# Kernel optimization log

Measured on AMD Instinct MI355X. Metric: run time of the kernel, lower is better.

Reference implementation:

```python
import jax, jax.numpy as jnp
import numpy as np

B, T, V, K = 8, 256, 16, 8
L_SRL, L_VN = 66, 40  # PropBank / VerbNet label inventory sizes


def setup_inputs() -> dict:
    key = jax.random.key(0)
    ks = jax.random.split(key, 7)
    log_srl = jax.random.normal(ks[0], (B, T, T, L_SRL), jnp.float32)
    log_vn = jax.random.normal(ks[1], (B, T, T, L_VN), jnp.float32)
    v_label = jax.random.randint(ks[2], (B, V), 0, T)          # predicate token positions
    v_l = jax.random.randint(ks[3], (B,), 1, V + 1)            # num predicates per example
    orig_l = jax.random.randint(ks[4], (B,), T // 2, T + 1)    # original seq lengths
    semlink = jax.random.randint(ks[5], (B, V, 2, K), 0, L_VN) # [.,.,0,:]=srl label ids, [.,.,1,:]=vn label ids
    semlink_l = jax.random.randint(ks[6], (B, V), 0, K + 1)    # num semlink constraints per predicate
    return {"log_srl": log_srl, "log_vn": log_vn, "v_label": v_label,
            "v_l": v_l, "orig_l": orig_l, "semlink": semlink, "semlink_l": semlink_l}


def reference(log_srl, log_vn, v_label, v_l, orig_l, semlink, semlink_l):
    # log_srl: [B,T,T,L_srl], log_vn: [B,T,T,L_vn]
    Bn, Tn = log_srl.shape[0], log_srl.shape[1]
    Vn, Kn = v_label.shape[1], semlink.shape[-1]
    b = jnp.arange(Bn)[:, None]
    # Gather predicate rows: [B,V,T,L]
    sel_srl = log_srl[b, v_label]
    sel_vn = log_vn[b, v_label]
    # batch_index1_select: gather along label axis with semlink label ids -> [B,V,T,K]
    r_idx = semlink[:, :, 0, :]  # [B,V,K]
    a_idx = semlink[:, :, 1, :]
    g_r = jnp.take_along_axis(sel_srl, r_idx[:, :, None, :], axis=3)
    g_a = jnp.take_along_axis(sel_vn, a_idx[:, :, None, :], axis=3)
    diff = jnp.abs(g_r - g_a)  # [B,V,T,K]
    # masks: semlink length (len_to_mask), valid predicates, valid tokens (:orig_l)
    k_mask = jnp.arange(Kn)[None, None, :] < semlink_l[:, :, None]   # [B,V,K]
    v_mask = jnp.arange(Vn)[None, :] < v_l[:, None]                  # [B,V]
    t_mask = jnp.arange(Tn)[None, :] < orig_l[:, None]               # [B,T]
    mask = (k_mask[:, :, None, :] & v_mask[:, :, None, None] & t_mask[:, None, :, None])
    loss = jnp.sum(jnp.where(mask, diff, 0.0))
    num_prop = jnp.sum(v_l).astype(log_srl.dtype)  # use_gold_predicate == 1 normalizer
    return loss / num_prop
```

## Files before the change

### kernel.cpp

```cpp
#include <hip/hip_runtime.h>

#define Bn   8
#define Tn   256
#define Vn   16
#define Kn   8
#define LSRL 66
#define LVN  40

#define SUM_SCALE 1073741824.0
#define SUM_MASK  ((1ULL << 56) - 1)
#define CNT_ONE   (1ULL << 56)
#define POISON    0xAAAAAAAAAAAAAAAAULL
#define POISON_END_CNT (((POISON >> 56) + 128) & 255ULL)

__global__ __launch_bounds__(256)
void semlink_onepass_kernel(const float* __restrict__ log_srl,
                            const float* __restrict__ log_vn,
                            const int*   __restrict__ v_label,
                            const int*   __restrict__ v_l,
                            const int*   __restrict__ orig_l,
                            const int*   __restrict__ semlink,
                            const int*   __restrict__ semlink_l,
                            unsigned long long* __restrict__ acc,
                            float*       __restrict__ out) {
    const int bv = blockIdx.x;
    const int b  = bv >> 4;
    const int v  = bv & 15;
    const int t  = threadIdx.x;
    const int lane = t & 63;
    const int wid  = t >> 6;

    __shared__ int s_idx[2 * Kn];
    __shared__ int s_meta[4];

    if (t < 2 * Kn) s_idx[t] = semlink[bv * (2 * Kn) + t];
    if (t == 0) {
        s_meta[0] = v_label[bv];
        s_meta[1] = semlink_l[bv];
        s_meta[2] = v_l[b];
        s_meta[3] = orig_l[b];
    }
    __syncthreads();

    const int label = s_meta[0];
    const int sl    = s_meta[1];
    const int vl    = s_meta[2];
    const int ol    = s_meta[3];

    float local = 0.0f;
    if (v < vl && t < ol) {
        const size_t row = ((size_t)b * Tn + label) * Tn + t;
        const float* srl_row = log_srl + row * LSRL;
        const float* vn_row  = log_vn  + row * LVN;
        #pragma unroll
        for (int k = 0; k < Kn; ++k) {
            if (k < sl) {
                local += fabsf(srl_row[s_idx[k]] - vn_row[s_idx[Kn + k]]);
            }
        }
    }

    #pragma unroll
    for (int off = 32; off > 0; off >>= 1) local += __shfl_down(local, off);

    __shared__ float wsum[4];
    if (lane == 0) wsum[wid] = local;
    __syncthreads();

    if (t == 0) {
        float bsum = (wsum[0] + wsum[1]) + (wsum[2] + wsum[3]);
        unsigned long long pack =
            CNT_ONE + (unsigned long long)((double)bsum * SUM_SCALE + 0.5);
        unsigned long long old =
            __hip_atomic_fetch_add(acc, pack, __ATOMIC_ACQ_REL,
                                   __HIP_MEMORY_SCOPE_AGENT);

        int np = 0;
        #pragma unroll
        for (int bb = 0; bb < Bn; ++bb) np += v_l[bb];

        if ((old >> 56) == 127ULL) {
            unsigned long long total = ((old & SUM_MASK) + (pack & SUM_MASK))
                                       & SUM_MASK;
            out[0] = (float)((double)total / SUM_SCALE / (double)np);
            __hip_atomic_store(acc, 0ULL, __ATOMIC_RELEASE,
                               __HIP_MEMORY_SCOPE_AGENT);
        } else if (old == POISON) {
            unsigned long long cur;
            do {
                cur = __hip_atomic_load(acc, __ATOMIC_ACQUIRE,
                                        __HIP_MEMORY_SCOPE_AGENT);
            } while ((cur >> 56) != POISON_END_CNT);
            unsigned long long total =
                (cur - POISON) & SUM_MASK;
            out[0] = (float)((double)total / SUM_SCALE / (double)np);
            __hip_atomic_store(acc, 0ULL, __ATOMIC_RELEASE,
                               __HIP_MEMORY_SCOPE_AGENT);
        }
    }
}

extern "C" void kernel_launch(void* const* d_in, const int* in_sizes, int n_in,
                              void* d_out, int out_size, void* d_ws, size_t ws_size,
                              hipStream_t stream) {
    const float* log_srl   = (const float*)d_in[0];
    const float* log_vn    = (const float*)d_in[1];
    const int*   v_label   = (const int*)d_in[2];
    const int*   v_l       = (const int*)d_in[3];
    const int*   orig_l    = (const int*)d_in[4];
    const int*   semlink   = (const int*)d_in[5];
    const int*   semlink_l = (const int*)d_in[6];
    float* out = (float*)d_out;
    unsigned long long* acc = (unsigned long long*)d_ws;

    semlink_onepass_kernel<<<Bn * Vn, Tn, 0, stream>>>(
        log_srl, log_vn, v_label, v_l, orig_l, semlink, semlink_l, acc, out);
}
```

Baseline: 10.83 us.

## Split work across 512 blocks with warps owning k-pairs and token quarters

Grid grows from 128 to 512 blocks: each block handles one quarter of the tokens for a (batch, predicate) pair, and each wavefront handles two of the eight semlink constraints. This spreads the latency-bound scattered gathers over more CUs and cuts the serial loads per thread. The shared-memory staging and its barrier are replaced by direct per-thread index loads. The packed atomic accumulator gets more count bits and a smaller fixed-point scale to track 512 arrivals, which lowers sum precision, and more blocks now contend on the single atomic.

```diff
diff --git a/kernel.cpp b/kernel.cpp
--- a/kernel.cpp
+++ b/kernel.cpp
@@ -7,11 +7,13 @@
 #define LSRL 66
 #define LVN  40
 
-#define SUM_SCALE 1073741824.0
-#define SUM_MASK  ((1ULL << 56) - 1)
-#define CNT_ONE   (1ULL << 56)
+#define NBLK      512
+#define SUM_SCALE 268435456.0
+#define CNT_SHIFT 52
+#define SUM_MASK  ((1ULL << CNT_SHIFT) - 1)
+#define CNT_ONE   (1ULL << CNT_SHIFT)
 #define POISON    0xAAAAAAAAAAAAAAAAULL
-#define POISON_END_CNT (((POISON >> 56) + 128) & 255ULL)
+#define POISON_END_CNT (((POISON >> CNT_SHIFT) + NBLK) & 4095ULL)
 
 __global__ __launch_bounds__(256)
 void semlink_onepass_kernel(const float* __restrict__ log_srl,
@@ -23,41 +25,34 @@
                             const int*   __restrict__ semlink_l,
                             unsigned long long* __restrict__ acc,
                             float*       __restrict__ out) {
-    const int bv = blockIdx.x;
-    const int b  = bv >> 4;
-    const int v  = bv & 15;
-    const int t  = threadIdx.x;
-    const int lane = t & 63;
-    const int wid  = t >> 6;
+    const int blk = blockIdx.x;
+    const int bv  = blk >> 2;
+    const int tq  = blk & 3;
+    const int b   = bv >> 4;
+    const int v   = bv & 15;
+    const int tid  = threadIdx.x;
+    const int lane = tid & 63;
+    const int wid  = tid >> 6;
+    const int t    = tq * 64 + lane;
+    const int kbase = wid * 2;
 
-    __shared__ int s_idx[2 * Kn];
-    __shared__ int s_meta[4];
-
-    if (t < 2 * Kn) s_idx[t] = semlink[bv * (2 * Kn) + t];
-    if (t == 0) {
-        s_meta[0] = v_label[bv];
-        s_meta[1] = semlink_l[bv];
-        s_meta[2] = v_l[b];
-        s_meta[3] = orig_l[b];
-    }
-    __syncthreads();
-
-    const int label = s_meta[0];
-    const int sl    = s_meta[1];
-    const int vl    = s_meta[2];
-    const int ol    = s_meta[3];
+    const int label = v_label[bv];
+    const int sl    = semlink_l[bv];
+    const int vl    = v_l[b];
+    const int ol    = orig_l[b];
+    const int* sl_base = semlink + bv * (2 * Kn);
+    const int r0 = sl_base[kbase];
+    const int r1 = sl_base[kbase + 1];
+    const int a0 = sl_base[Kn + kbase];
+    const int a1 = sl_base[Kn + kbase + 1];
 
     float local = 0.0f;
     if (v < vl && t < ol) {
         const size_t row = ((size_t)b * Tn + label) * Tn + t;
         const float* srl_row = log_srl + row * LSRL;
         const float* vn_row  = log_vn  + row * LVN;
-        #pragma unroll
-        for (int k = 0; k < Kn; ++k) {
-            if (k < sl) {
-                local += fabsf(srl_row[s_idx[k]] - vn_row[s_idx[Kn + k]]);
-            }
-        }
+        if (kbase     < sl) local += fabsf(srl_row[r0] - vn_row[a0]);
+        if (kbase + 1 < sl) local += fabsf(srl_row[r1] - vn_row[a1]);
     }
 
     #pragma unroll
@@ -67,7 +62,7 @@
     if (lane == 0) wsum[wid] = local;
     __syncthreads();
 
-    if (t == 0) {
+    if (tid == 0) {
         float bsum = (wsum[0] + wsum[1]) + (wsum[2] + wsum[3]);
         unsigned long long pack =
             CNT_ONE + (unsigned long long)((double)bsum * SUM_SCALE + 0.5);
@@ -79,9 +74,9 @@
         #pragma unroll
         for (int bb = 0; bb < Bn; ++bb) np += v_l[bb];
 
-        if ((old >> 56) == 127ULL) {
-            unsigned long long total = ((old & SUM_MASK) + (pack & SUM_MASK))
-                                       & SUM_MASK;
+        if ((old >> CNT_SHIFT) == (unsigned long long)(NBLK - 1)) {
+            unsigned long long total =
+                ((old & SUM_MASK) + (pack & SUM_MASK)) & SUM_MASK;
             out[0] = (float)((double)total / SUM_SCALE / (double)np);
             __hip_atomic_store(acc, 0ULL, __ATOMIC_RELEASE,
                                __HIP_MEMORY_SCOPE_AGENT);
@@ -90,9 +85,8 @@
             do {
                 cur = __hip_atomic_load(acc, __ATOMIC_ACQUIRE,
                                         __HIP_MEMORY_SCOPE_AGENT);
-            } while ((cur >> 56) != POISON_END_CNT);
-            unsigned long long total =
-                (cur - POISON) & SUM_MASK;
+            } while ((cur >> CNT_SHIFT) != POISON_END_CNT);
+            unsigned long long total = (cur - POISON) & SUM_MASK;
             out[0] = (float)((double)total / SUM_SCALE / (double)np);
             __hip_atomic_store(acc, 0ULL, __ATOMIC_RELEASE,
                                __HIP_MEMORY_SCOPE_AGENT);
@@ -113,6 +107,6 @@
     float* out = (float*)d_out;
     unsigned long long* acc = (unsigned long long*)d_ws;
 
-    semlink_onepass_kernel<<<Bn * Vn, Tn, 0, stream>>>(
+    semlink_onepass_kernel<<<NBLK, 256, 0, stream>>>(
         log_srl, log_vn, v_label, v_l, orig_l, semlink, semlink_l, acc, out);
 }
```

New measurement: 15.77 us. 45.6% more time.
